# Performance work log

Hardware: AMD Instinct MI355X
Metric: run time of the kernel (lower is better)

Reference implementation:

```python
import jax, jax.numpy as jnp
import numpy as np

B, S, D, H, DFF = 2, 2048, 512, 8, 2048
DK = D // H
EPS = 1e-6  # LayerNormalization eps


def _ln(x, a, b):
    # torch: alpha * (x - mean) / (std + eps) + bias, std is unbiased (ddof=1)
    m = jnp.mean(x, axis=-1, keepdims=True)
    s = jnp.std(x, axis=-1, keepdims=True, ddof=1)
    return a * (x - m) / (s + EPS) + b


def _mha(Q, K, V, mask, Wq, bq, Wk, bk, Wv, bv, Wo, bo):
    Bq, Sq = Q.shape[0], Q.shape[1]
    Sk = K.shape[1]
    q = (Q @ Wq + bq).reshape(Bq, Sq, H, DK).transpose(0, 2, 1, 3)  # bhqd
    k = (K @ Wk + bk).reshape(Bq, Sk, H, DK).transpose(0, 2, 1, 3)  # bhkd
    v = (V @ Wv + bv).reshape(Bq, Sk, H, DK).transpose(0, 2, 1, 3)  # bhkd
    scores = jnp.einsum('bhqd,bhkd->bhqk', q, k) / jnp.sqrt(jnp.float32(DK))
    scores = jnp.where(mask == 0, -jnp.inf, scores)  # masked_fill(mask==0, -inf)
    attn = jax.nn.softmax(scores, axis=-1)  # dropout is identity in eval
    out = jnp.einsum('bhqk,bhkd->bhqd', attn, v)
    out = out.transpose(0, 2, 1, 3).reshape(Bq, Sq, D)
    return out @ Wo + bo


def setup_inputs() -> dict:
    key = jax.random.key(0)
    ks = jax.random.split(key, 20)
    sc = 0.02
    inp = {
        'x': jax.random.normal(ks[0], (B, S, D), jnp.float32),
        'encoder_output': jax.random.normal(ks[1], (B, S, D), jnp.float32),
        'encoder_output_mask': jnp.broadcast_to(jnp.ones((S, S), jnp.int32), (B, 1, S, S)),
        'decoder_mask': jnp.broadcast_to(jnp.tril(jnp.ones((S, S), jnp.int32)), (B, 1, S, S)),
        'sa_Wq': jax.random.normal(ks[2], (D, D), jnp.float32) * sc,
        'sa_bq': jnp.zeros((D,), jnp.float32),
        'sa_Wk': jax.random.normal(ks[3], (D, D), jnp.float32) * sc,
        'sa_bk': jnp.zeros((D,), jnp.float32),
        'sa_Wv': jax.random.normal(ks[4], (D, D), jnp.float32) * sc,
        'sa_bv': jnp.zeros((D,), jnp.float32),
        'sa_Wo': jax.random.normal(ks[5], (D, D), jnp.float32) * sc,
        'sa_bo': jnp.zeros((D,), jnp.float32),
        'ca_Wq': jax.random.normal(ks[6], (D, D), jnp.float32) * sc,
        'ca_bq': jnp.zeros((D,), jnp.float32),
        'ca_Wk': jax.random.normal(ks[7], (D, D), jnp.float32) * sc,
        'ca_bk': jnp.zeros((D,), jnp.float32),
        'ca_Wv': jax.random.normal(ks[8], (D, D), jnp.float32) * sc,
        'ca_bv': jnp.zeros((D,), jnp.float32),
        'ca_Wo': jax.random.normal(ks[9], (D, D), jnp.float32) * sc,
        'ca_bo': jnp.zeros((D,), jnp.float32),
        'ff_W1': jax.random.normal(ks[10], (D, DFF), jnp.float32) * sc,
        'ff_b1': jnp.zeros((DFF,), jnp.float32),
        'ff_W2': jax.random.normal(ks[11], (DFF, D), jnp.float32) * sc,
        'ff_b2': jnp.zeros((D,), jnp.float32),
        'ln0_a': jnp.ones((1,), jnp.float32), 'ln0_b': jnp.zeros((1,), jnp.float32),
        'ln1_a': jnp.ones((1,), jnp.float32), 'ln1_b': jnp.zeros((1,), jnp.float32),
        'ln2_a': jnp.ones((1,), jnp.float32), 'ln2_b': jnp.zeros((1,), jnp.float32),
    }
    return inp


def reference(x, encoder_output, encoder_output_mask, decoder_mask,
              sa_Wq, sa_bq, sa_Wk, sa_bk, sa_Wv, sa_bv, sa_Wo, sa_bo,
              ca_Wq, ca_bq, ca_Wk, ca_bk, ca_Wv, ca_bv, ca_Wo, ca_bo,
              ff_W1, ff_b1, ff_W2, ff_b2,
              ln0_a, ln0_b, ln1_a, ln1_b, ln2_a, ln2_b):
    # Residual 0: pre-norm self-attention (dropout = identity in eval)
    n = _ln(x, ln0_a, ln0_b)
    x = x + _mha(n, n, n, decoder_mask, sa_Wq, sa_bq, sa_Wk, sa_bk, sa_Wv, sa_bv, sa_Wo, sa_bo)
    # Residual 1: pre-norm cross-attention
    n = _ln(x, ln1_a, ln1_b)
    x = x + _mha(n, encoder_output, encoder_output, encoder_output_mask,
                 ca_Wq, ca_bq, ca_Wk, ca_bk, ca_Wv, ca_bv, ca_Wo, ca_bo)
    # Residual 2: pre-norm FFN (Linear -> ReLU -> Linear)
    n = _ln(x, ln2_a, ln2_b)
    x = x + (jax.nn.relu(n @ ff_W1 + ff_b1) @ ff_W2 + ff_b2)
    return x
```

## Files before the change

kernel.cpp:

```cpp
#include <hip/hip_runtime.h>
#include <hip/hip_bf16.h>

typedef __bf16 bf16_t;
typedef __bf16 bf16x8_t __attribute__((ext_vector_type(8)));
typedef float f32x4_t __attribute__((ext_vector_type(4)));

static constexpr int B_ = 2, S_ = 2048, D_ = 512, H_ = 8, DK_ = 64, DFF_ = 2048;
static constexpr int M_ = B_ * S_;

__device__ __forceinline__ unsigned pkbf(float a, float b) {
  union { bf16_t h; unsigned short u; } x, y;
  x.h = (bf16_t)a; y.h = (bf16_t)b;
  return (unsigned)x.u | ((unsigned)y.u << 16);
}

__device__ __forceinline__ void async16(bf16_t* lds, const bf16_t* g) {
  __builtin_amdgcn_global_load_lds((__attribute__((address_space(1))) void*)g,
                                   (__attribute__((address_space(3))) void*)lds,
                                   16, 0, 0);
}

__global__ __launch_bounds__(256) void ln_kernel(const float* __restrict__ x,
                                                 const float* __restrict__ ga,
                                                 const float* __restrict__ gb,
                                                 bf16_t* __restrict__ out) {
  const int row = blockIdx.x * 4 + (threadIdx.x >> 6);
  const int lane = threadIdx.x & 63;
  const float4* xr = (const float4*)(x + (long)row * D_);
  float4 v0 = xr[lane * 2];
  float4 v1 = xr[lane * 2 + 1];
  float s = v0.x + v0.y + v0.z + v0.w + v1.x + v1.y + v1.z + v1.w;
  float ss = v0.x * v0.x + v0.y * v0.y + v0.z * v0.z + v0.w * v0.w +
             v1.x * v1.x + v1.y * v1.y + v1.z * v1.z + v1.w * v1.w;
#pragma unroll
  for (int m = 1; m < 64; m <<= 1) {
    s += __shfl_xor(s, m);
    ss += __shfl_xor(ss, m);
  }
  const float mean = s * (1.0f / 512.0f);
  float var = (ss - 512.0f * mean * mean) * (1.0f / 511.0f);
  var = fmaxf(var, 0.0f);
  const float sc = ga[0] / (sqrtf(var) + 1e-6f);
  const float sh = gb[0] - mean * sc;
  alignas(16) bf16_t y[8];
  y[0] = (bf16_t)(v0.x * sc + sh);
  y[1] = (bf16_t)(v0.y * sc + sh);
  y[2] = (bf16_t)(v0.z * sc + sh);
  y[3] = (bf16_t)(v0.w * sc + sh);
  y[4] = (bf16_t)(v1.x * sc + sh);
  y[5] = (bf16_t)(v1.y * sc + sh);
  y[6] = (bf16_t)(v1.z * sc + sh);
  y[7] = (bf16_t)(v1.w * sc + sh);
  ((uint4*)(out + (long)row * D_))[lane] = *(uint4*)y;
}

__global__ __launch_bounds__(256) void cvt_bf16(const float* __restrict__ x,
                                                bf16_t* __restrict__ y) {
  const long i = ((long)blockIdx.x * 256 + threadIdx.x) * 8;
  float4 a = *(const float4*)(x + i);
  float4 b = *(const float4*)(x + i + 4);
  alignas(16) bf16_t t[8];
  t[0] = (bf16_t)a.x; t[1] = (bf16_t)a.y; t[2] = (bf16_t)a.z; t[3] = (bf16_t)a.w;
  t[4] = (bf16_t)b.x; t[5] = (bf16_t)b.y; t[6] = (bf16_t)b.z; t[7] = (bf16_t)b.w;
  *(uint4*)(y + i) = *(uint4*)t;
}

__device__ __forceinline__ void wtrans_body(const float* __restrict__ W,
                                            bf16_t* __restrict__ Wt, int K, int N,
                                            int k0, int n0) {
  constexpr int LDT = 65;
  __shared__ float T[64 * LDT];
  const int tid = threadIdx.x;
#pragma unroll
  for (int p = 0; p < 4; ++p) {
    int e = p * 1024 + tid * 4;
    int kr = e >> 6, nc = e & 63;
    float4 f = *(const float4*)(W + (long)(k0 + kr) * N + n0 + nc);
    T[kr * LDT + nc + 0] = f.x;
    T[kr * LDT + nc + 1] = f.y;
    T[kr * LDT + nc + 2] = f.z;
    T[kr * LDT + nc + 3] = f.w;
  }
  __syncthreads();
#pragma unroll
  for (int p = 0; p < 4; ++p) {
    int e = p * 1024 + tid * 4;
    int nr = e >> 6, kc = e & 63;
    alignas(8) bf16_t t[4];
#pragma unroll
    for (int j = 0; j < 4; ++j) t[j] = (bf16_t)T[(kc + j) * LDT + nr];
    *(uint2*)(Wt + (long)(n0 + nr) * K + k0 + kc) = *(uint2*)t;
  }
}

__global__ __launch_bounds__(256) void wtrans(const float* __restrict__ W,
                                              bf16_t* __restrict__ Wt, int K, int N) {
  wtrans_body(W, Wt, K, N, blockIdx.x * 64, blockIdx.y * 64);
}

struct WT8 { const float* W[8]; bf16_t* T[8]; };
__global__ __launch_bounds__(256) void wtrans8(WT8 a) {
  wtrans_body(a.W[blockIdx.z], a.T[blockIdx.z], 512, 512,
              blockIdx.x * 64, blockIdx.y * 64);
}

__global__ __launch_bounds__(256) void vtrans(const bf16_t* __restrict__ v,
                                              bf16_t* __restrict__ vt) {
  constexpr int LDT = 66;
  __shared__ bf16_t T[64 * LDT];
  const int tid = threadIdx.x;
  const int bh = blockIdx.y, b = bh >> 3, h = bh & 7;
  const int s0 = blockIdx.x * 64;
#pragma unroll
  for (int p = 0; p < 2; ++p) {
    int e = p * 2048 + tid * 8;
    int sr = e >> 6, c = e & 63;
    uint4 u = *(const uint4*)(v + (long)(b * S_ + s0 + sr) * D_ + h * DK_ + c);
    bf16_t* pv = (bf16_t*)&u;
#pragma unroll
    for (int j = 0; j < 8; ++j) T[(c + j) * LDT + sr] = pv[j];
  }
  __syncthreads();
#pragma unroll
  for (int p = 0; p < 2; ++p) {
    int e = p * 2048 + tid * 8;
    int d = e >> 6, sc = e & 63;
    alignas(16) bf16_t t[8];
#pragma unroll
    for (int j = 0; j < 8; ++j) t[j] = T[d * LDT + sc + j];
    *(uint4*)(vt + ((long)bh * DK_ + d) * S_ + s0 + sc) = *(uint4*)t;
  }
}

struct GArg {
  const bf16_t* A;
  const bf16_t* Wt;
  const float* bias;
  const float* res;
  void* out;
};

template <int BN, int MODE>
__global__ __launch_bounds__(256, 2) void gemm_bt(GArg g0, GArg g1, GArg g2,
                                                  int M, int N, int K) {
  constexpr int WAVES_N = BN / 64;
  constexpr int WAVES_M = 4 / WAVES_N;
  constexpr int WM = 128 / WAVES_M;
  constexpr int AI = WM / 16;
  __shared__ bf16_t As[2][128 * 32];
  __shared__ bf16_t Bs[2][BN * 32];
  GArg g = (blockIdx.z == 0) ? g0 : (blockIdx.z == 1) ? g1 : g2;
  const int tid = threadIdx.x;
  const int wave = tid >> 6, lane = tid & 63, quad = lane >> 4, l15 = lane & 15;
  const long m0 = (long)blockIdx.x * 128;
  const long n0 = (long)blockIdx.y * BN;
  const int wm = (wave / WAVES_N) * WM;
  const int wn = (wave % WAVES_N) * 64;

  const int r4 = lane >> 2;
  const int cg = (lane & 3) ^ ((lane >> 3) & 3);
  const bf16_t* Ab = g.A + m0 * (long)K + cg * 8;
  const bf16_t* Bb = g.Wt + n0 * (long)K + cg * 8;

  auto stage = [&](int buf, int k0) {
#pragma unroll
    for (int c = 0; c < 2; ++c) {
      const int row = wave * 32 + c * 16;
      async16(&As[buf][row * 32], Ab + (long)(row + r4) * K + k0);
    }
    if constexpr (BN == 128) {
#pragma unroll
      for (int c = 0; c < 2; ++c) {
        const int row = wave * 32 + c * 16;
        async16(&Bs[buf][row * 32], Bb + (long)(row + r4) * K + k0);
      }
    } else {
      const int row = wave * 16;
      async16(&Bs[buf][row * 32], Bb + (long)(row + r4) * K + k0);
    }
  };

  f32x4_t acc[AI][4];
#pragma unroll
  for (int i = 0; i < AI; ++i)
#pragma unroll
    for (int j = 0; j < 4; ++j) acc[i][j] = (f32x4_t){0.f, 0.f, 0.f, 0.f};

  const int KT = K >> 5;
  const int sc = quad ^ ((l15 >> 1) & 3);
  stage(0, 0);
  for (int kt = 0; kt < KT; ++kt) {
    __syncthreads();
    if (kt + 1 < KT) stage((kt + 1) & 1, (kt + 1) * 32);
    const bf16_t* Al = &As[kt & 1][0];
    const bf16_t* Bl = &Bs[kt & 1][0];
    bf16x8_t af[AI], bfr[4];
#pragma unroll
    for (int i = 0; i < AI; ++i)
      af[i] = *(const bf16x8_t*)&Al[(wm + i * 16 + l15) * 32 + sc * 8];
#pragma unroll
    for (int j = 0; j < 4; ++j)
      bfr[j] = *(const bf16x8_t*)&Bl[(wn + j * 16 + l15) * 32 + sc * 8];
#pragma unroll
    for (int i = 0; i < AI; ++i)
#pragma unroll
      for (int j = 0; j < 4; ++j)
        acc[i][j] = __builtin_amdgcn_mfma_f32_16x16x32_bf16(af[i], bfr[j], acc[i][j], 0, 0, 0);
  }

#pragma unroll
  for (int i = 0; i < AI; ++i) {
#pragma unroll
    for (int j = 0; j < 4; ++j) {
      const long col = n0 + wn + j * 16 + l15;
      const float bv = g.bias[col];
#pragma unroll
      for (int r = 0; r < 4; ++r) {
        const long row = m0 + wm + i * 16 + quad * 4 + r;
        float v = acc[i][j][r] + bv;
        if constexpr (MODE == 1) v = fmaxf(v, 0.f);
        if constexpr (MODE == 2) {
          ((float*)g.out)[row * N + col] = v + g.res[row * N + col];
        } else {
          ((bf16_t*)g.out)[row * N + col] = (bf16_t)v;
        }
      }
    }
  }
}

template <bool CAUSAL>
__global__ __launch_bounds__(256, 2) void flash_attn(const bf16_t* __restrict__ Q,
                                                     const bf16_t* __restrict__ Kg,
                                                     const bf16_t* __restrict__ Vt,
                                                     bf16_t* __restrict__ O) {
  __shared__ bf16_t Ks[2][64 * 64];
  __shared__ bf16_t Vs[2][64 * 64];
  constexpr int LDP = 72;
  __shared__ bf16_t Ps[4][16 * LDP];
  const int tid = threadIdx.x, wave = tid >> 6, lane = tid & 63;
  const int quad = lane >> 4, l15 = lane & 15;
  const int bh = blockIdx.y, b = bh >> 3, h = bh & 7;
  const int q0 = blockIdx.x * 64;
  const int qw = q0 + wave * 16;
  const long base = (long)b * S_ * D_ + (long)h * DK_;
  const long vtbase = (long)bh * DK_ * S_;

  const bf16_t* Qp = Q + base + (long)(qw + l15) * D_ + quad * 8;
  const bf16x8_t qf0 = *(const bf16x8_t*)(Qp);
  const bf16x8_t qf1 = *(const bf16x8_t*)(Qp + 32);

  const int r8 = lane >> 3;
  const int cg8 = (lane & 7) ^ r8;
  const bf16_t* Kb = Kg + base + cg8 * 8;
  const bf16_t* Vb = Vt + vtbase + cg8 * 8;

  auto stage = [&](int buf, int kk0) {
#pragma unroll
    for (int c = 0; c < 2; ++c) {
      const int row = wave * 16 + c * 8;
      async16(&Ks[buf][row * 64], Kb + (long)(kk0 + row + r8) * D_);
      async16(&Vs[buf][row * 64], Vb + (long)(row + r8) * S_ + kk0);
    }
  };

  float mi = -1e30f, li = 0.f;
  f32x4_t o[4];
#pragma unroll
  for (int db = 0; db < 4; ++db) o[db] = (f32x4_t){0.f, 0.f, 0.f, 0.f};

  const int nt = CAUSAL ? (blockIdx.x + 1) : (S_ >> 6);
  bf16_t* Pw = &Ps[wave][0];

  stage(0, 0);
  for (int t = 0; t < nt; ++t) {
    __syncthreads();
    if (t + 1 < nt) stage((t + 1) & 1, (t + 1) * 64);
    const bf16_t* Kt = &Ks[t & 1][0];
    const bf16_t* Vl = &Vs[t & 1][0];
    const int kk0 = t * 64;

    f32x4_t st[4];
#pragma unroll
    for (int nb = 0; nb < 4; ++nb) {
      f32x4_t a = (f32x4_t){0.f, 0.f, 0.f, 0.f};
#pragma unroll
      for (int ks = 0; ks < 2; ++ks) {
        const int scf = (ks * 4 + quad) ^ (l15 & 7);
        const bf16x8_t kf = *(const bf16x8_t*)&Kt[(nb * 16 + l15) * 64 + scf * 8];
        a = __builtin_amdgcn_mfma_f32_16x16x32_bf16(kf, ks ? qf1 : qf0, a, 0, 0, 0);
      }
      st[nb] = a;
    }

    const bool domask = CAUSAL && (kk0 + 63 > qw);
    float mx = -1e30f;
#pragma unroll
    for (int nb = 0; nb < 4; ++nb)
#pragma unroll
      for (int r = 0; r < 4; ++r) {
        float v = st[nb][r] * 0.125f;
        if (domask && (kk0 + nb * 16 + quad * 4 + r > qw + l15)) v = -1e30f;
        st[nb][r] = v;
        mx = fmaxf(mx, v);
      }
    mx = fmaxf(mx, __shfl_xor(mx, 16));
    mx = fmaxf(mx, __shfl_xor(mx, 32));
    const float mnew = fmaxf(mi, mx);
    float sum = 0.f;
#pragma unroll
    for (int nb = 0; nb < 4; ++nb)
#pragma unroll
      for (int r = 0; r < 4; ++r) {
        float p = __expf(st[nb][r] - mnew);
        st[nb][r] = p;
        sum += p;
      }
    sum += __shfl_xor(sum, 16);
    sum += __shfl_xor(sum, 32);
    const float alpha = __expf(mi - mnew);
    mi = mnew;
    li = li * alpha + sum;
#pragma unroll
    for (int db = 0; db < 4; ++db)
#pragma unroll
      for (int r = 0; r < 4; ++r) o[db][r] *= alpha;

#pragma unroll
    for (int nb = 0; nb < 4; ++nb) {
      uint2 w;
      w.x = pkbf(st[nb][0], st[nb][1]);
      w.y = pkbf(st[nb][2], st[nb][3]);
      *(uint2*)&Pw[l15 * LDP + nb * 16 + quad * 4] = w;
    }
    const bf16x8_t pf0 = *(const bf16x8_t*)&Pw[l15 * LDP + 0 + quad * 8];
    const bf16x8_t pf1 = *(const bf16x8_t*)&Pw[l15 * LDP + 32 + quad * 8];
#pragma unroll
    for (int ks = 0; ks < 2; ++ks) {
      const bf16x8_t pf = ks ? pf1 : pf0;
#pragma unroll
      for (int db = 0; db < 4; ++db) {
        const int scf = (ks * 4 + quad) ^ (l15 & 7);
        const bf16x8_t vf = *(const bf16x8_t*)&Vl[(db * 16 + l15) * 64 + scf * 8];
        o[db] = __builtin_amdgcn_mfma_f32_16x16x32_bf16(vf, pf, o[db], 0, 0, 0);
      }
    }
  }

  const float inv = 1.0f / li;
#pragma unroll
  for (int db = 0; db < 4; ++db) {
    uint2 w;
    w.x = pkbf(o[db][0] * inv, o[db][1] * inv);
    w.y = pkbf(o[db][2] * inv, o[db][3] * inv);
    *(uint2*)(O + base + (long)(qw + l15) * D_ + db * 16 + quad * 4) = w;
  }
}

extern "C" void kernel_launch(void* const* d_in, const int* in_sizes, int n_in,
                              void* d_out, int out_size, void* d_ws, size_t ws_size,
                              hipStream_t stream) {
  const float* x    = (const float*)d_in[0];
  const float* enc  = (const float*)d_in[1];
  const float* saWq = (const float*)d_in[4];  const float* sabq = (const float*)d_in[5];
  const float* saWk = (const float*)d_in[6];  const float* sabk = (const float*)d_in[7];
  const float* saWv = (const float*)d_in[8];  const float* sabv = (const float*)d_in[9];
  const float* saWo = (const float*)d_in[10]; const float* sabo = (const float*)d_in[11];
  const float* caWq = (const float*)d_in[12]; const float* cabq = (const float*)d_in[13];
  const float* caWk = (const float*)d_in[14]; const float* cabk = (const float*)d_in[15];
  const float* caWv = (const float*)d_in[16]; const float* cabv = (const float*)d_in[17];
  const float* caWo = (const float*)d_in[18]; const float* cabo = (const float*)d_in[19];
  const float* ffW1 = (const float*)d_in[20]; const float* ffb1 = (const float*)d_in[21];
  const float* ffW2 = (const float*)d_in[22]; const float* ffb2 = (const float*)d_in[23];
  const float* ln0a = (const float*)d_in[24]; const float* ln0b = (const float*)d_in[25];
  const float* ln1a = (const float*)d_in[26]; const float* ln1b = (const float*)d_in[27];
  const float* ln2a = (const float*)d_in[28]; const float* ln2b = (const float*)d_in[29];

  char* ws = (char*)d_ws;
  size_t off = 0;
  auto alloc = [&](size_t bytes) -> void* {
    void* p = ws + off;
    off += (bytes + 255) & ~(size_t)255;
    return p;
  };
  bf16_t* wt_saq = (bf16_t*)alloc(512 * 512 * 2);
  bf16_t* wt_sak = (bf16_t*)alloc(512 * 512 * 2);
  bf16_t* wt_sav = (bf16_t*)alloc(512 * 512 * 2);
  bf16_t* wt_sao = (bf16_t*)alloc(512 * 512 * 2);
  bf16_t* wt_caq = (bf16_t*)alloc(512 * 512 * 2);
  bf16_t* wt_cak = (bf16_t*)alloc(512 * 512 * 2);
  bf16_t* wt_cav = (bf16_t*)alloc(512 * 512 * 2);
  bf16_t* wt_cao = (bf16_t*)alloc(512 * 512 * 2);
  bf16_t* wt_f1  = (bf16_t*)alloc((size_t)512 * 2048 * 2);
  bf16_t* wt_f2  = (bf16_t*)alloc((size_t)2048 * 512 * 2);
  bf16_t* enc_b  = (bf16_t*)alloc((size_t)M_ * D_ * 2);
  bf16_t* nbuf   = (bf16_t*)alloc((size_t)M_ * D_ * 2);
  bf16_t* qb     = (bf16_t*)alloc((size_t)M_ * D_ * 2);
  bf16_t* kb     = (bf16_t*)alloc((size_t)M_ * D_ * 2);
  bf16_t* vb     = (bf16_t*)alloc((size_t)M_ * D_ * 2);
  bf16_t* vtb    = (bf16_t*)alloc((size_t)M_ * D_ * 2);
  bf16_t* attnb  = (bf16_t*)alloc((size_t)M_ * D_ * 2);
  bf16_t* hid    = (bf16_t*)alloc((size_t)M_ * DFF_ * 2);
  float*  x1     = (float*)alloc((size_t)M_ * D_ * 4);
  float*  x2     = (float*)alloc((size_t)M_ * D_ * 4);

  {
    WT8 a;
    a.W[0] = saWq; a.T[0] = wt_saq;
    a.W[1] = saWk; a.T[1] = wt_sak;
    a.W[2] = saWv; a.T[2] = wt_sav;
    a.W[3] = saWo; a.T[3] = wt_sao;
    a.W[4] = caWq; a.T[4] = wt_caq;
    a.W[5] = caWk; a.T[5] = wt_cak;
    a.W[6] = caWv; a.T[6] = wt_cav;
    a.W[7] = caWo; a.T[7] = wt_cao;
    wtrans8<<<dim3(8, 8, 8), 256, 0, stream>>>(a);
  }
  wtrans<<<dim3(8, 32), 256, 0, stream>>>(ffW1, wt_f1, 512, 2048);
  wtrans<<<dim3(32, 8), 256, 0, stream>>>(ffW2, wt_f2, 2048, 512);
  cvt_bf16<<<1024, 256, 0, stream>>>(enc, enc_b);

  ln_kernel<<<1024, 256, 0, stream>>>(x, ln0a, ln0b, nbuf);
  {
    GArg z0{nbuf, wt_saq, sabq, nullptr, qb};
    GArg z1{nbuf, wt_sak, sabk, nullptr, kb};
    GArg z2{nbuf, wt_sav, sabv, nullptr, vb};
    gemm_bt<128, 0><<<dim3(32, 4, 3), 256, 0, stream>>>(z0, z1, z2, M_, 512, 512);
  }
  vtrans<<<dim3(32, 16), 256, 0, stream>>>(vb, vtb);
  flash_attn<true><<<dim3(32, 16), 256, 0, stream>>>(qb, kb, vtb, attnb);
  {
    GArg o1{attnb, wt_sao, sabo, x, x1};
    gemm_bt<64, 2><<<dim3(32, 8, 1), 256, 0, stream>>>(o1, o1, o1, M_, 512, 512);
  }

  ln_kernel<<<1024, 256, 0, stream>>>(x1, ln1a, ln1b, nbuf);
  {
    GArg c0{nbuf,  wt_caq, cabq, nullptr, qb};
    GArg c1{enc_b, wt_cak, cabk, nullptr, kb};
    GArg c2{enc_b, wt_cav, cabv, nullptr, vb};
    gemm_bt<128, 0><<<dim3(32, 4, 3), 256, 0, stream>>>(c0, c1, c2, M_, 512, 512);
  }
  vtrans<<<dim3(32, 16), 256, 0, stream>>>(vb, vtb);
  flash_attn<false><<<dim3(32, 16), 256, 0, stream>>>(qb, kb, vtb, attnb);
  {
    GArg o2{attnb, wt_cao, cabo, x1, x2};
    gemm_bt<64, 2><<<dim3(32, 8, 1), 256, 0, stream>>>(o2, o2, o2, M_, 512, 512);
  }

  ln_kernel<<<1024, 256, 0, stream>>>(x2, ln2a, ln2b, nbuf);
  {
    GArg f1{nbuf, wt_f1, ffb1, nullptr, hid};
    gemm_bt<128, 1><<<dim3(32, 16, 1), 256, 0, stream>>>(f1, f1, f1, M_, DFF_, 512);
  }
  {
    GArg f2{hid, wt_f2, ffb2, x2, d_out};
    gemm_bt<64, 2><<<dim3(32, 8, 1), 256, 0, stream>>>(f2, f2, f2, M_, 512, DFF_);
  }
}
```

Before: 399.5 us.

## Split attention KV range across two chunks, shrink GEMM tiles, fold softmax scale into Q

Flash attention now splits each query tile's key range into two chunks along a new grid dimension. Each chunk writes unnormalized fp32 partial outputs plus row max and sum, and a new merge kernel combines them into bf16. Causal tiles are processed in reverse order to balance load. GEMMs move to 64-row tiles with a 2x2 wave layout and higher occupancy bounds, giving more blocks per launch. The 1/sqrt(dk)*log2(e) factor is folded into the Q projection epilogue so the softmax uses exp2. The costs are an extra kernel launch, fp32 partial traffic (reusing the hidden buffer), and less reuse per GEMM tile.

Measured after the change: 392.5 us. Within noise of the previous version (-1.8%).

```diff
diff --git a/kernel.cpp b/kernel.cpp
--- a/kernel.cpp
+++ b/kernel.cpp
@@ -7,6 +7,7 @@
 
 static constexpr int B_ = 2, S_ = 2048, D_ = 512, H_ = 8, DK_ = 64, DFF_ = 2048;
 static constexpr int M_ = B_ * S_;
+static constexpr float QSCALE = 0.125f * 1.44269504f;
 
 __device__ __forceinline__ unsigned pkbf(float a, float b) {
   union { bf16_t h; unsigned short u; } x, y;
@@ -138,24 +139,24 @@
   const float* bias;
   const float* res;
   void* out;
+  float oscale;
 };
 
-template <int BN, int MODE>
-__global__ __launch_bounds__(256, 2) void gemm_bt(GArg g0, GArg g1, GArg g2,
+template <int BM, int BN, int MODE>
+__global__ __launch_bounds__(256, 4) void gemm_bt(GArg g0, GArg g1, GArg g2,
                                                   int M, int N, int K) {
-  constexpr int WAVES_N = BN / 64;
-  constexpr int WAVES_M = 4 / WAVES_N;
-  constexpr int WM = 128 / WAVES_M;
-  constexpr int AI = WM / 16;
-  __shared__ bf16_t As[2][128 * 32];
+  constexpr int WM = BM / 2, WN = BN / 2;
+  constexpr int AI = WM / 16, BJ = WN / 16;
+  constexpr int RA = BM / 64, RB = BN / 64;
+  __shared__ bf16_t As[2][BM * 32];
   __shared__ bf16_t Bs[2][BN * 32];
   GArg g = (blockIdx.z == 0) ? g0 : (blockIdx.z == 1) ? g1 : g2;
   const int tid = threadIdx.x;
   const int wave = tid >> 6, lane = tid & 63, quad = lane >> 4, l15 = lane & 15;
-  const long m0 = (long)blockIdx.x * 128;
+  const long m0 = (long)blockIdx.x * BM;
   const long n0 = (long)blockIdx.y * BN;
-  const int wm = (wave / WAVES_N) * WM;
-  const int wn = (wave % WAVES_N) * 64;
+  const int wm = (wave >> 1) * WM;
+  const int wn = (wave & 1) * WN;
 
   const int r4 = lane >> 2;
   const int cg = (lane & 3) ^ ((lane >> 3) & 3);
@@ -164,27 +165,22 @@
 
   auto stage = [&](int buf, int k0) {
 #pragma unroll
-    for (int c = 0; c < 2; ++c) {
-      const int row = wave * 32 + c * 16;
+    for (int c = 0; c < RA; ++c) {
+      const int row = c * 64 + wave * 16;
       async16(&As[buf][row * 32], Ab + (long)(row + r4) * K + k0);
     }
-    if constexpr (BN == 128) {
-#pragma unroll
-      for (int c = 0; c < 2; ++c) {
-        const int row = wave * 32 + c * 16;
-        async16(&Bs[buf][row * 32], Bb + (long)(row + r4) * K + k0);
-      }
-    } else {
-      const int row = wave * 16;
+#pragma unroll
+    for (int c = 0; c < RB; ++c) {
+      const int row = c * 64 + wave * 16;
       async16(&Bs[buf][row * 32], Bb + (long)(row + r4) * K + k0);
     }
   };
 
-  f32x4_t acc[AI][4];
+  f32x4_t acc[AI][BJ];
 #pragma unroll
   for (int i = 0; i < AI; ++i)
 #pragma unroll
-    for (int j = 0; j < 4; ++j) acc[i][j] = (f32x4_t){0.f, 0.f, 0.f, 0.f};
+    for (int j = 0; j < BJ; ++j) acc[i][j] = (f32x4_t){0.f, 0.f, 0.f, 0.f};
 
   const int KT = K >> 5;
   const int sc = quad ^ ((l15 >> 1) & 3);
@@ -194,24 +190,24 @@
     if (kt + 1 < KT) stage((kt + 1) & 1, (kt + 1) * 32);
     const bf16_t* Al = &As[kt & 1][0];
     const bf16_t* Bl = &Bs[kt & 1][0];
-    bf16x8_t af[AI], bfr[4];
+    bf16x8_t af[AI], bfr[BJ];
 #pragma unroll
     for (int i = 0; i < AI; ++i)
       af[i] = *(const bf16x8_t*)&Al[(wm + i * 16 + l15) * 32 + sc * 8];
 #pragma unroll
-    for (int j = 0; j < 4; ++j)
+    for (int j = 0; j < BJ; ++j)
       bfr[j] = *(const bf16x8_t*)&Bl[(wn + j * 16 + l15) * 32 + sc * 8];
 #pragma unroll
     for (int i = 0; i < AI; ++i)
 #pragma unroll
-      for (int j = 0; j < 4; ++j)
+      for (int j = 0; j < BJ; ++j)
         acc[i][j] = __builtin_amdgcn_mfma_f32_16x16x32_bf16(af[i], bfr[j], acc[i][j], 0, 0, 0);
   }
 
 #pragma unroll
   for (int i = 0; i < AI; ++i) {
 #pragma unroll
-    for (int j = 0; j < 4; ++j) {
+    for (int j = 0; j < BJ; ++j) {
       const long col = n0 + wn + j * 16 + l15;
       const float bv = g.bias[col];
 #pragma unroll
@@ -222,7 +218,7 @@
         if constexpr (MODE == 2) {
           ((float*)g.out)[row * N + col] = v + g.res[row * N + col];
         } else {
-          ((bf16_t*)g.out)[row * N + col] = (bf16_t)v;
+          ((bf16_t*)g.out)[row * N + col] = (bf16_t)(v * g.oscale);
         }
       }
     }
@@ -230,10 +226,12 @@
 }
 
 template <bool CAUSAL>
-__global__ __launch_bounds__(256, 2) void flash_attn(const bf16_t* __restrict__ Q,
+__global__ __launch_bounds__(256, 3) void flash_attn(const bf16_t* __restrict__ Q,
                                                      const bf16_t* __restrict__ Kg,
                                                      const bf16_t* __restrict__ Vt,
-                                                     bf16_t* __restrict__ O) {
+                                                     float* __restrict__ po,
+                                                     float* __restrict__ pm,
+                                                     float* __restrict__ pl) {
   __shared__ bf16_t Ks[2][64 * 64];
   __shared__ bf16_t Vs[2][64 * 64];
   constexpr int LDP = 72;
@@ -241,7 +239,23 @@
   const int tid = threadIdx.x, wave = tid >> 6, lane = tid & 63;
   const int quad = lane >> 4, l15 = lane & 15;
   const int bh = blockIdx.y, b = bh >> 3, h = bh & 7;
-  const int q0 = blockIdx.x * 64;
+  const int qt = CAUSAL ? (31 - (int)blockIdx.x) : (int)blockIdx.x;
+  const int chunk = blockIdx.z;
+  const int ntt = CAUSAL ? (qt + 1) : 32;
+  const int n0t = (ntt + 1) >> 1;
+  const int tstart = chunk ? n0t : 0;
+  const int tend = chunk ? ntt : n0t;
+  const long pbase = ((long)chunk * 16 + bh) * 32 + qt;
+
+  if (tstart >= tend) {
+#pragma unroll
+    for (int i = 0; i < 4; ++i)
+      *(f32x4_t*)&po[pbase * 4096 + tid * 16 + i * 4] = (f32x4_t){0.f, 0.f, 0.f, 0.f};
+    if (tid < 64) { pm[pbase * 64 + tid] = -1e30f; pl[pbase * 64 + tid] = 0.f; }
+    return;
+  }
+
+  const int q0 = qt * 64;
   const int qw = q0 + wave * 16;
   const long base = (long)b * S_ * D_ + (long)h * DK_;
   const long vtbase = (long)bh * DK_ * S_;
@@ -255,7 +269,8 @@
   const bf16_t* Kb = Kg + base + cg8 * 8;
   const bf16_t* Vb = Vt + vtbase + cg8 * 8;
 
-  auto stage = [&](int buf, int kk0) {
+  auto stage = [&](int buf, int t) {
+    const int kk0 = t * 64;
 #pragma unroll
     for (int c = 0; c < 2; ++c) {
       const int row = wave * 16 + c * 8;
@@ -269,15 +284,15 @@
 #pragma unroll
   for (int db = 0; db < 4; ++db) o[db] = (f32x4_t){0.f, 0.f, 0.f, 0.f};
 
-  const int nt = CAUSAL ? (blockIdx.x + 1) : (S_ >> 6);
   bf16_t* Pw = &Ps[wave][0];
 
-  stage(0, 0);
-  for (int t = 0; t < nt; ++t) {
+  stage(0, tstart);
+  for (int t = tstart; t < tend; ++t) {
+    const int buf = (t - tstart) & 1;
     __syncthreads();
-    if (t + 1 < nt) stage((t + 1) & 1, (t + 1) * 64);
-    const bf16_t* Kt = &Ks[t & 1][0];
-    const bf16_t* Vl = &Vs[t & 1][0];
+    if (t + 1 < tend) stage(buf ^ 1, t + 1);
+    const bf16_t* Kt = &Ks[buf][0];
+    const bf16_t* Vl = &Vs[buf][0];
     const int kk0 = t * 64;
 
     f32x4_t st[4];
@@ -293,13 +308,13 @@
       st[nb] = a;
     }
 
-    const bool domask = CAUSAL && (kk0 + 63 > qw);
+    const bool domask = CAUSAL && (t == qt);
     float mx = -1e30f;
 #pragma unroll
     for (int nb = 0; nb < 4; ++nb)
 #pragma unroll
       for (int r = 0; r < 4; ++r) {
-        float v = st[nb][r] * 0.125f;
+        float v = st[nb][r];
         if (domask && (kk0 + nb * 16 + quad * 4 + r > qw + l15)) v = -1e30f;
         st[nb][r] = v;
         mx = fmaxf(mx, v);
@@ -312,13 +327,13 @@
     for (int nb = 0; nb < 4; ++nb)
 #pragma unroll
       for (int r = 0; r < 4; ++r) {
-        float p = __expf(st[nb][r] - mnew);
+        float p = exp2f(st[nb][r] - mnew);
         st[nb][r] = p;
         sum += p;
       }
     sum += __shfl_xor(sum, 16);
     sum += __shfl_xor(sum, 32);
-    const float alpha = __expf(mi - mnew);
+    const float alpha = exp2f(mi - mnew);
     mi = mnew;
     li = li * alpha + sum;
 #pragma unroll
@@ -347,14 +362,43 @@
     }
   }
 
-  const float inv = 1.0f / li;
-#pragma unroll
-  for (int db = 0; db < 4; ++db) {
-    uint2 w;
-    w.x = pkbf(o[db][0] * inv, o[db][1] * inv);
-    w.y = pkbf(o[db][2] * inv, o[db][3] * inv);
-    *(uint2*)(O + base + (long)(qw + l15) * D_ + db * 16 + quad * 4) = w;
-  }
+#pragma unroll
+  for (int db = 0; db < 4; ++db)
+    *(f32x4_t*)&po[pbase * 4096 + (wave * 16 + l15) * 64 + db * 16 + quad * 4] = o[db];
+  if (quad == 0) {
+    pm[pbase * 64 + wave * 16 + l15] = mi;
+    pl[pbase * 64 + wave * 16 + l15] = li;
+  }
+}
+
+__global__ __launch_bounds__(256) void merge_attn(const float* __restrict__ po,
+                                                  const float* __restrict__ pm,
+                                                  const float* __restrict__ pl,
+                                                  bf16_t* __restrict__ O) {
+  const int qt = blockIdx.x, bh = blockIdx.y, b = bh >> 3, h = bh & 7;
+  const long p0 = ((long)bh) * 32 + qt;
+  const long p1 = ((long)16 + bh) * 32 + qt;
+  const int t = threadIdx.x;
+  const int q = t >> 2, d0 = (t & 3) * 16;
+  const float m0 = pm[p0 * 64 + q], m1 = pm[p1 * 64 + q];
+  const float l0 = pl[p0 * 64 + q], l1 = pl[p1 * 64 + q];
+  const float m = fmaxf(m0, m1);
+  const float a0 = exp2f(m0 - m), a1 = exp2f(m1 - m);
+  const float inv = 1.0f / (l0 * a0 + l1 * a1);
+  const float s0 = a0 * inv, s1 = a1 * inv;
+  const long i0 = p0 * 4096 + q * 64 + d0;
+  const long i1 = p1 * 4096 + q * 64 + d0;
+  alignas(16) bf16_t out[16];
+#pragma unroll
+  for (int j = 0; j < 4; ++j) {
+    f32x4_t a = *(const f32x4_t*)&po[i0 + j * 4];
+    f32x4_t c = *(const f32x4_t*)&po[i1 + j * 4];
+#pragma unroll
+    for (int r = 0; r < 4; ++r) out[j * 4 + r] = (bf16_t)(a[r] * s0 + c[r] * s1);
+  }
+  const long row = (long)b * S_ + qt * 64 + q;
+  *(uint4*)(O + row * D_ + h * DK_ + d0) = *(uint4*)&out[0];
+  *(uint4*)(O + row * D_ + h * DK_ + d0 + 8) = *(uint4*)&out[8];
 }
 
 extern "C" void kernel_launch(void* const* d_in, const int* in_sizes, int n_in,
@@ -403,6 +447,9 @@
   bf16_t* hid    = (bf16_t*)alloc((size_t)M_ * DFF_ * 2);
   float*  x1     = (float*)alloc((size_t)M_ * D_ * 4);
   float*  x2     = (float*)alloc((size_t)M_ * D_ * 4);
+  float*  pm     = (float*)alloc(2 * 16 * 32 * 64 * 4);
+  float*  pl     = (float*)alloc(2 * 16 * 32 * 64 * 4);
+  float*  po     = (float*)hid;
 
   {
     WT8 a;
@@ -422,39 +469,41 @@
 
   ln_kernel<<<1024, 256, 0, stream>>>(x, ln0a, ln0b, nbuf);
   {
-    GArg z0{nbuf, wt_saq, sabq, nullptr, qb};
-    GArg z1{nbuf, wt_sak, sabk, nullptr, kb};
-    GArg z2{nbuf, wt_sav, sabv, nullptr, vb};
-    gemm_bt<128, 0><<<dim3(32, 4, 3), 256, 0, stream>>>(z0, z1, z2, M_, 512, 512);
+    GArg z0{nbuf, wt_saq, sabq, nullptr, qb, QSCALE};
+    GArg z1{nbuf, wt_sak, sabk, nullptr, kb, 1.0f};
+    GArg z2{nbuf, wt_sav, sabv, nullptr, vb, 1.0f};
+    gemm_bt<64, 64, 0><<<dim3(64, 8, 3), 256, 0, stream>>>(z0, z1, z2, M_, 512, 512);
   }
   vtrans<<<dim3(32, 16), 256, 0, stream>>>(vb, vtb);
-  flash_attn<true><<<dim3(32, 16), 256, 0, stream>>>(qb, kb, vtb, attnb);
-  {
-    GArg o1{attnb, wt_sao, sabo, x, x1};
-    gemm_bt<64, 2><<<dim3(32, 8, 1), 256, 0, stream>>>(o1, o1, o1, M_, 512, 512);
+  flash_attn<true><<<dim3(32, 16, 2), 256, 0, stream>>>(qb, kb, vtb, po, pm, pl);
+  merge_attn<<<dim3(32, 16), 256, 0, stream>>>(po, pm, pl, attnb);
+  {
+    GArg o1{attnb, wt_sao, sabo, x, x1, 1.0f};
+    gemm_bt<64, 64, 2><<<dim3(64, 8, 1), 256, 0, stream>>>(o1, o1, o1, M_, 512, 512);
   }
 
   ln_kernel<<<1024, 256, 0, stream>>>(x1, ln1a, ln1b, nbuf);
   {
-    GArg c0{nbuf,  wt_caq, cabq, nullptr, qb};
-    GArg c1{enc_b, wt_cak, cabk, nullptr, kb};
-    GArg c2{enc_b, wt_cav, cabv, nullptr, vb};
-    gemm_bt<128, 0><<<dim3(32, 4, 3), 256, 0, stream>>>(c0, c1, c2, M_, 512, 512);
+    GArg c0{nbuf,  wt_caq, cabq, nullptr, qb, QSCALE};
+    GArg c1{enc_b, wt_cak, cabk, nullptr, kb, 1.0f};
+    GArg c2{enc_b, wt_cav, cabv, nullptr, vb, 1.0f};
+    gemm_bt<64, 64, 0><<<dim3(64, 8, 3), 256, 0, stream>>>(c0, c1, c2, M_, 512, 512);
   }
   vtrans<<<dim3(32, 16), 256, 0, stream>>>(vb, vtb);
-  flash_attn<false><<<dim3(32, 16), 256, 0, stream>>>(qb, kb, vtb, attnb);
-  {
-    GArg o2{attnb, wt_cao, cabo, x1, x2};
-    gemm_bt<64, 2><<<dim3(32, 8, 1), 256, 0, stream>>>(o2, o2, o2, M_, 512, 512);
+  flash_attn<false><<<dim3(32, 16, 2), 256, 0, stream>>>(qb, kb, vtb, po, pm, pl);
+  merge_attn<<<dim3(32, 16), 256, 0, stream>>>(po, pm, pl, attnb);
+  {
+    GArg o2{attnb, wt_cao, cabo, x1, x2, 1.0f};
+    gemm_bt<64, 64, 2><<<dim3(64, 8, 1), 256, 0, stream>>>(o2, o2, o2, M_, 512, 512);
   }
 
   ln_kernel<<<1024, 256, 0, stream>>>(x2, ln2a, ln2b, nbuf);
   {
-    GArg f1{nbuf, wt_f1, ffb1, nullptr, hid};
-    gemm_bt<128, 1><<<dim3(32, 16, 1), 256, 0, stream>>>(f1, f1, f1, M_, DFF_, 512);
-  }
-  {
-    GArg f2{hid, wt_f2, ffb2, x2, d_out};
-    gemm_bt<64, 2><<<dim3(32, 8, 1), 256, 0, stream>>>(f2, f2, f2, M_, 512, DFF_);
-  }
-}
+    GArg f1{nbuf, wt_f1, ffb1, nullptr, hid, 1.0f};
+    gemm_bt<64, 128, 1><<<dim3(64, 16, 1), 256, 0, stream>>>(f1, f1, f1, M_, DFF_, 512);
+  }
+  {
+    GArg f2{hid, wt_f2, ffb2, x2, d_out, 1.0f};
+    gemm_bt<64, 64, 2><<<dim3(64, 8, 1), 256, 0, stream>>>(f2, f2, f2, M_, 512, DFF_);
+  }
+}
```
